# Performance work log

Hardware: AMD Instinct MI355X
Metric: run time of the kernel (lower is better)

Reference implementation:

```python
import jax, jax.numpy as jnp
import numpy as np

B, N, H = 8, 2048, 1024

def setup_inputs() -> dict:
    key = jax.random.key(0)
    ks = jax.random.split(key, 10)
    s = 1.0 / np.sqrt(2 * H)
    return {
        "sem": jax.random.normal(ks[0], (B, N, H), jnp.float32),
        "temp": jax.random.normal(ks[1], (B, N, H), jnp.float32),
        "Wq": jax.random.normal(ks[2], (2 * H, H), jnp.float32) * s,
        "bq": jnp.zeros((H,), jnp.float32),
        "Wk": jax.random.normal(ks[3], (2 * H, H), jnp.float32) * s,
        "bk": jnp.zeros((H,), jnp.float32),
        "Wv": jax.random.normal(ks[4], (2 * H, H), jnp.float32) * s,
        "bv": jnp.zeros((H,), jnp.float32),
        "Wg": jax.random.normal(ks[5], (2 * H, 1), jnp.float32) * s,
        "bg": jnp.zeros((1,), jnp.float32),
    }

def reference(sem, temp, Wq, bq, Wk, bk, Wv, bv, Wg, bg):
    combined = jnp.concatenate([sem, temp], axis=-1)          # [B,N,2H]
    Q = combined @ Wq + bq                                    # [B,N,H]
    K = combined @ Wk + bk
    V = combined @ Wv + bv
    scale = 1.0 / jnp.sqrt(jnp.asarray(Q.shape[-1], Q.dtype))
    scores = jnp.einsum('bqh,bkh->bqk', Q, K) * scale         # [B,N,N]
    attn = jax.nn.softmax(scores, axis=-1)
    gate = jax.nn.sigmoid(combined @ Wg + bg)                 # [B,N,1]
    attn_weights = attn * gate                                # row-wise gate
    fused = jnp.einsum('bqk,bkh->bqh', attn_weights, V)       # [B,N,H]
    return fused + sem, attn_weights.mean(axis=1)             # [B,N,H], [B,N]
```

## Files before the change

### kernel.cpp

```cpp
#include <hip/hip_runtime.h>
#include <stdint.h>
#include <math.h>

#define NB 8
#define NN 2048
#define HH 1024
#define K2 2048
#define MM 16384

typedef unsigned short u16;
typedef __attribute__((ext_vector_type(8))) short short8v;
typedef __attribute__((ext_vector_type(4))) float floatx4;

__device__ __forceinline__ float bf2f(u16 u) { return __uint_as_float(((unsigned)u) << 16); }
__device__ __forceinline__ u16 f2bf(float f) {
  unsigned u = __float_as_uint(f);
  unsigned r = (u + 0x7fffu + ((u >> 16) & 1u)) >> 16;
  return (u16)r;
}

__device__ __forceinline__ void async16(const void* g, void* lds) {
  __builtin_amdgcn_global_load_lds((const __attribute__((address_space(1))) void*)g,
                                   (__attribute__((address_space(3))) void*)lds,
                                   16, 0, 0);
}

__device__ __forceinline__ int xcd_swz(int bid, int nblk) {
  return (bid & 7) * (nblk >> 3) + (bid >> 3);
}

__device__ __forceinline__ void gemm256_core(const u16* __restrict__ A, int lda,
                                             const u16* __restrict__ Bt, int ldb,
                                             int rowA0, int rowB0, int K,
                                             u16* sA, u16* sB, floatx4 acc[8][4]) {
  const int t = threadIdx.x;
  const int w = t >> 6, l = t & 63;
  const int wr = w >> 2, wc = w & 3;

#pragma unroll
  for (int mi = 0; mi < 8; mi++)
#pragma unroll
    for (int ni = 0; ni < 4; ni++) { floatx4 z = {0.f,0.f,0.f,0.f}; acc[mi][ni] = z; }

  const int cS = ((t & 3) ^ ((t >> 3) & 3)) << 3;
  const u16* gA0 = A + (size_t)(rowA0 + (t >> 2)) * lda + cS;
  const u16* gA1 = A + (size_t)(rowA0 + 128 + (t >> 2)) * lda + cS;
  const u16* gB0 = Bt + (size_t)(rowB0 + (t >> 2)) * ldb + cS;
  const u16* gB1 = Bt + (size_t)(rowB0 + 128 + (t >> 2)) * ldb + cS;
  char* dA = (char*)sA + (w << 10) + (l << 4);
  char* dB = (char*)sB + (w << 10) + (l << 4);

  const int fr = l & 15;
  const int xr = (fr >> 1) & 3;
  const int ch = ((l >> 4) ^ xr) << 4;
  const int abase = (wr * 128 + fr) * 64 + ch;
  const int bbase = (wc * 64 + fr) * 64 + ch;

  const int NTt = K >> 5;

#define STG(bi, kt) { const int ko_ = (kt) << 5;                       \
    char* dA_ = dA + (bi) * 16384; char* dB_ = dB + (bi) * 16384;      \
    async16(gA0 + ko_, dA_);        async16(gA1 + ko_, dA_ + 8192);    \
    async16(gB0 + ko_, dB_);        async16(gB1 + ko_, dB_ + 8192); }

  STG(0, 0);
  STG(1, 1);

  int bc = 0, bs = 2;
  for (int tt = 0; tt < NTt; ++tt) {
    if (tt < NTt - 1) { asm volatile("s_waitcnt vmcnt(4)" ::: "memory"); }
    else              { asm volatile("s_waitcnt vmcnt(0)" ::: "memory"); }
    __builtin_amdgcn_s_barrier();
    if (tt + 2 < NTt) STG(bs, tt + 2);

    const char* a = (const char*)sA + bc * 16384;
    const char* b = (const char*)sB + bc * 16384;
    short8v bfr[4], afr[8];
#pragma unroll
    for (int ni = 0; ni < 4; ni++) bfr[ni] = *(const short8v*)(b + bbase + ni * 1024);
#pragma unroll
    for (int mi = 0; mi < 8; mi++) afr[mi] = *(const short8v*)(a + abase + mi * 1024);
    __builtin_amdgcn_s_setprio(1);
#pragma unroll
    for (int mi = 0; mi < 8; mi++)
#pragma unroll
      for (int ni = 0; ni < 4; ni++)
        acc[mi][ni] = __builtin_amdgcn_mfma_f32_16x16x32_bf16(afr[mi], bfr[ni], acc[mi][ni], 0, 0, 0);
    __builtin_amdgcn_s_setprio(0);
    bc = (bc == 2) ? 0 : bc + 1;
    bs = (bs == 2) ? 0 : bs + 1;
  }
#undef STG
}

__global__ void __launch_bounds__(256) k_prep_x(const float* __restrict__ sem,
                                                const float* __restrict__ temp,
                                                u16* __restrict__ X) {
  size_t i = (((size_t)blockIdx.x * 256) + threadIdx.x) << 2;
  int row = (int)(i >> 11);
  int col = (int)(i & 2047);
  const float* src = (col < 1024) ? (sem + (size_t)row * 1024 + col)
                                  : (temp + (size_t)row * 1024 + (col - 1024));
  float4 v = *(const float4*)src;
  ushort4 o;
  o.x = f2bf(v.x); o.y = f2bf(v.y); o.z = f2bf(v.z); o.w = f2bf(v.w);
  *(ushort4*)(X + i) = o;
}

__global__ void __launch_bounds__(256) k_transpose_w(const float* __restrict__ W,
                                                     u16* __restrict__ Wt) {
  __shared__ float s[32][33];
  int tile = blockIdx.x;
  int nt = tile & 31, kt = tile >> 5;
  int tx = threadIdx.x & 31, ty = threadIdx.x >> 5;
  int n0 = nt << 5, k0 = kt << 5;
#pragma unroll
  for (int j = 0; j < 32; j += 8)
    s[ty + j][tx] = W[(size_t)(k0 + ty + j) * 1024 + (n0 + tx)];
  __syncthreads();
#pragma unroll
  for (int j = 0; j < 32; j += 8)
    Wt[(size_t)(n0 + ty + j) * 2048 + (k0 + tx)] = f2bf(s[tx][ty + j]);
}

__global__ void __launch_bounds__(512, 2) k_proj_qkv(const u16* __restrict__ X,
                                                     const u16* __restrict__ Wt,
                                                     const float* __restrict__ bq,
                                                     const float* __restrict__ bk,
                                                     const float* __restrict__ bv,
                                                     u16* __restrict__ Qb,
                                                     u16* __restrict__ Kb,
                                                     u16* __restrict__ Vt) {
  __shared__ __align__(16) u16 sA[3 * 8192];
  __shared__ __align__(16) u16 sB[3 * 8192];
  int tile = xcd_swz(blockIdx.x, 768);
  int bm = tile / 12, bn = tile - bm * 12;
  floatx4 acc[8][4];
  gemm256_core(X, K2, Wt, K2, bm * 256, bn * 256, K2, sA, sB, acc);

  const int t = threadIdx.x, w = t >> 6, l = t & 63;
  const int wr = w >> 2, wc = w & 3;
  const int r0 = bm * 256 + wr * 128 + ((l >> 4) << 2);
  const int cg0 = bn * 256 + wc * 64 + (l & 15);
  const int which = bn >> 2;
  const float* bias = which == 0 ? bq : which == 1 ? bk : bv;
#pragma unroll
  for (int ni = 0; ni < 4; ni++) {
    int c1 = (cg0 + ni * 16) & 1023;
    float bvv = bias[c1];
#pragma unroll
    for (int mi = 0; mi < 8; mi++)
#pragma unroll
      for (int i = 0; i < 4; i++) {
        int rg = r0 + mi * 16 + i;
        u16 ob = f2bf(acc[mi][ni][i] + bvv);
        if (which == 0)      Qb[(size_t)rg * 1024 + c1] = ob;
        else if (which == 1) Kb[(size_t)rg * 1024 + c1] = ob;
        else                 Vt[((size_t)(rg >> 11) * 1024 + c1) * 2048 + (rg & 2047)] = ob;
      }
  }
}

__global__ void __launch_bounds__(256) k_gate(const u16* __restrict__ X, const float* __restrict__ Wg,
                                              const float* __restrict__ bg, float* __restrict__ gate) {
  int row = blockIdx.x * 4 + (threadIdx.x >> 6);
  int l = threadIdx.x & 63;
  const short* xr = (const short*)(X + (size_t)row * 2048);
  float s = 0.f;
#pragma unroll
  for (int i = 0; i < 4; i++) {
    int k = i * 512 + l * 8;
    short8v v = *(const short8v*)&xr[k];
#pragma unroll
    for (int j = 0; j < 8; j++) s += bf2f((u16)v[j]) * Wg[k + j];
  }
#pragma unroll
  for (int off = 32; off > 0; off >>= 1) s += __shfl_xor(s, off);
  if (l == 0) gate[row] = 1.f / (1.f + expf(-(s + bg[0])));
}

__global__ void __launch_bounds__(512, 2) k_scores(const u16* __restrict__ Q, const u16* __restrict__ Kb,
                                                   u16* __restrict__ E, float* __restrict__ lsum) {
  __shared__ __align__(16) u16 sA[3 * 8192];
  __shared__ __align__(16) u16 sB[3 * 8192];
  int tile = xcd_swz(blockIdx.x, 512);
  int b = tile >> 6, r = tile & 63, bm = r >> 3, bn = r & 7;
  const u16* A = Q + (size_t)b * NN * HH;
  const u16* Bt = Kb + (size_t)b * NN * HH;
  floatx4 acc[8][4];
  gemm256_core(A, HH, Bt, HH, bm * 256, bn * 256, HH, sA, sB, acc);

  u16* Eb = E + (size_t)b * NN * NN;
  float* lb = lsum + b * NN;
  const int t = threadIdx.x, w = t >> 6, l = t & 63;
  const int wr = w >> 2, wc = w & 3;
  const int q0 = bm * 256 + wr * 128 + ((l >> 4) << 2);
  const int k0c = bn * 256 + wc * 64 + (l & 15);
#pragma unroll
  for (int mi = 0; mi < 8; mi++)
#pragma unroll
    for (int i = 0; i < 4; i++) {
      int q = q0 + mi * 16 + i;
      float rs = 0.f;
#pragma unroll
      for (int ni = 0; ni < 4; ni++) {
        float e = expf(acc[mi][ni][i] * 0.03125f);
        Eb[(size_t)q * NN + k0c + ni * 16] = f2bf(e);
        rs += e;
      }
      rs += __shfl_xor(rs, 1);
      rs += __shfl_xor(rs, 2);
      rs += __shfl_xor(rs, 4);
      rs += __shfl_xor(rs, 8);
      if ((l & 15) == 0) atomicAdd(&lb[q], rs);
    }
}

__global__ void __launch_bounds__(512, 2) k_pv(const u16* __restrict__ E, const u16* __restrict__ Vt,
                                               const float* __restrict__ gate, const float* __restrict__ lsum,
                                               const float* __restrict__ sem, float* __restrict__ out) {
  __shared__ __align__(16) u16 sA[3 * 8192];
  __shared__ __align__(16) u16 sB[3 * 8192];
  int tile = xcd_swz(blockIdx.x, 256);
  int b = tile >> 5, r = tile & 31, bm = r >> 2, bn = r & 3;
  const u16* A = E + (size_t)b * NN * NN;
  const u16* Bt = Vt + (size_t)b * HH * NN;
  floatx4 acc[8][4];
  gemm256_core(A, NN, Bt, NN, bm * 256, bn * 256, NN, sA, sB, acc);

  const int t = threadIdx.x, w = t >> 6, l = t & 63;
  const int wr = w >> 2, wc = w & 3;
  const int q0 = bm * 256 + wr * 128 + ((l >> 4) << 2);
  const int h0 = bn * 256 + wc * 64 + (l & 15);
#pragma unroll
  for (int mi = 0; mi < 8; mi++)
#pragma unroll
    for (int i = 0; i < 4; i++) {
      int q = q0 + mi * 16 + i;
      size_t gq = (size_t)b * NN + q;
      float wq = gate[gq] / lsum[gq];
#pragma unroll
      for (int ni = 0; ni < 4; ni++) {
        int h = h0 + ni * 16;
        out[gq * HH + h] = acc[mi][ni][i] * wq + sem[gq * HH + h];
      }
    }
}

__global__ void __launch_bounds__(256) k_colmean(const u16* __restrict__ E, const float* __restrict__ gate,
                                                 const float* __restrict__ lsum, float* __restrict__ cm) {
  __shared__ float wsh[256];
  int bid = blockIdx.x;
  int b = bid >> 6, rest = bid & 63;
  int ks = rest >> 3, qc = rest & 7;
  int t = threadIdx.x;
  {
    size_t gq = (size_t)b * NN + qc * 256 + t;
    wsh[t] = gate[gq] / lsum[gq];
  }
  __syncthreads();
  int k = ks * 256 + t;
  const u16* Eb = E + ((size_t)b * NN + (size_t)qc * 256) * NN + k;
  float s = 0.f;
  for (int q = 0; q < 256; q++) s += wsh[q] * bf2f(Eb[(size_t)q * NN]);
  atomicAdd(&cm[b * NN + k], s * (1.f / 2048.f));
}

extern "C" void kernel_launch(void* const* d_in, const int* in_sizes, int n_in,
                              void* d_out, int out_size, void* d_ws, size_t ws_size,
                              hipStream_t stream) {
  const float* sem  = (const float*)d_in[0];
  const float* temp = (const float*)d_in[1];
  const float* Wq   = (const float*)d_in[2];
  const float* bq   = (const float*)d_in[3];
  const float* Wk   = (const float*)d_in[4];
  const float* bk   = (const float*)d_in[5];
  const float* Wv   = (const float*)d_in[6];
  const float* bv   = (const float*)d_in[7];
  const float* Wg   = (const float*)d_in[8];
  const float* bg   = (const float*)d_in[9];
  float* out = (float*)d_out;

  char* ws = (char*)d_ws;
  u16* X      = (u16*)ws;
  u16* E      = X;
  u16* WqkvT  = (u16*)(ws + 67108864);
  u16* Qb     = (u16*)(ws + 79691776);
  u16* Kb     = (u16*)(ws + 113246208);
  u16* Vt     = (u16*)(ws + 146800640);
  float* gate = (float*)(ws + 180355072);
  float* lsum = (float*)(ws + 180420608);

  hipMemsetAsync(lsum, 0, 65536, stream);
  hipMemsetAsync(out + 16777216, 0, 65536, stream);

  k_prep_x<<<32768, 256, 0, stream>>>(sem, temp, X);
  k_transpose_w<<<2048, 256, 0, stream>>>(Wq, WqkvT);
  k_transpose_w<<<2048, 256, 0, stream>>>(Wk, WqkvT + (size_t)1024 * 2048);
  k_transpose_w<<<2048, 256, 0, stream>>>(Wv, WqkvT + (size_t)2048 * 2048);
  k_proj_qkv<<<768, 512, 0, stream>>>(X, WqkvT, bq, bk, bv, Qb, Kb, Vt);
  k_gate<<<4096, 256, 0, stream>>>(X, Wg, bg, gate);
  k_scores<<<512, 512, 0, stream>>>(Qb, Kb, E, lsum);
  k_pv<<<256, 512, 0, stream>>>(E, Vt, gate, lsum, sem, out);
  k_colmean<<<512, 256, 0, stream>>>(E, gate, lsum, out + 16777216);
}
```

Before: 580.4 us.

## Switch GEMMs to 128x128 tiles with double buffering and fuse gate into prep

Replaces the 256x256, 512-thread, triple-buffered GEMM core with a 128x128, 256-thread, double-buffered core that has an extra barrier each iteration. The projection, scores and PV kernels get more, smaller blocks so more of them can run per CU. The gate computation moves into the bf16 conversion kernel and uses fp32 inputs, removing a separate pass over X. V is stored transposed with vectorized ushort4 writes. Smaller tiles lower per-block data reuse and raise global and LDS traffic per FLOP, and the shallower pipeline may expose load latency.

```diff
diff --git a/kernel.cpp b/kernel.cpp
--- a/kernel.cpp
+++ b/kernel.cpp
@@ -29,82 +29,101 @@
   return (bid & 7) * (nblk >> 3) + (bid >> 3);
 }
 
-__device__ __forceinline__ void gemm256_core(const u16* __restrict__ A, int lda,
+#define SBAR() __builtin_amdgcn_sched_barrier(0)
+
+__device__ __forceinline__ void gemm128_core(const u16* __restrict__ A, int lda,
                                              const u16* __restrict__ Bt, int ldb,
                                              int rowA0, int rowB0, int K,
-                                             u16* sA, u16* sB, floatx4 acc[8][4]) {
+                                             u16* sA, u16* sB, floatx4 acc[4][4]) {
   const int t = threadIdx.x;
   const int w = t >> 6, l = t & 63;
-  const int wr = w >> 2, wc = w & 3;
-
-#pragma unroll
-  for (int mi = 0; mi < 8; mi++)
+  const int wr = w >> 1, wc = w & 1;
+
+#pragma unroll
+  for (int mi = 0; mi < 4; mi++)
 #pragma unroll
     for (int ni = 0; ni < 4; ni++) { floatx4 z = {0.f,0.f,0.f,0.f}; acc[mi][ni] = z; }
 
-  const int cS = ((t & 3) ^ ((t >> 3) & 3)) << 3;
-  const u16* gA0 = A + (size_t)(rowA0 + (t >> 2)) * lda + cS;
-  const u16* gA1 = A + (size_t)(rowA0 + 128 + (t >> 2)) * lda + cS;
-  const u16* gB0 = Bt + (size_t)(rowB0 + (t >> 2)) * ldb + cS;
-  const u16* gB1 = Bt + (size_t)(rowB0 + 128 + (t >> 2)) * ldb + cS;
-  char* dA = (char*)sA + (w << 10) + (l << 4);
-  char* dB = (char*)sB + (w << 10) + (l << 4);
+  const int srow = l >> 2;
+  const int cs = (((l & 3) ^ ((l >> 3) & 3)) << 3);
+  const u16* gA0 = A + (size_t)(rowA0 + w * 32 + srow) * lda + cs;
+  const u16* gA1 = A + (size_t)(rowA0 + w * 32 + 16 + srow) * lda + cs;
+  const u16* gB0 = Bt + (size_t)(rowB0 + w * 32 + srow) * ldb + cs;
+  const u16* gB1 = Bt + (size_t)(rowB0 + w * 32 + 16 + srow) * ldb + cs;
+  char* dA = (char*)sA + w * 2048 + l * 16;
+  char* dB = (char*)sB + w * 2048 + l * 16;
 
   const int fr = l & 15;
-  const int xr = (fr >> 1) & 3;
-  const int ch = ((l >> 4) ^ xr) << 4;
-  const int abase = (wr * 128 + fr) * 64 + ch;
-  const int bbase = (wc * 64 + fr) * 64 + ch;
-
-  const int NTt = K >> 5;
-
-#define STG(bi, kt) { const int ko_ = (kt) << 5;                       \
-    char* dA_ = dA + (bi) * 16384; char* dB_ = dB + (bi) * 16384;      \
-    async16(gA0 + ko_, dA_);        async16(gA1 + ko_, dA_ + 8192);    \
-    async16(gB0 + ko_, dB_);        async16(gB1 + ko_, dB_ + 8192); }
-
-  STG(0, 0);
-  STG(1, 1);
-
-  int bc = 0, bs = 2;
-  for (int tt = 0; tt < NTt; ++tt) {
-    if (tt < NTt - 1) { asm volatile("s_waitcnt vmcnt(4)" ::: "memory"); }
-    else              { asm volatile("s_waitcnt vmcnt(0)" ::: "memory"); }
+  const int ch = (((l >> 4) ^ ((fr >> 1) & 3)) << 4);
+  const int abase = wr * 4096 + fr * 64 + ch;
+  const int bbase = wc * 4096 + fr * 64 + ch;
+
+  const int NT = K >> 5;
+
+#define STG128(bi, kt) { const int ko_ = (kt) << 5; const int bo_ = (bi) << 13; \
+    async16(gA0 + ko_, dA + bo_); async16(gA1 + ko_, dA + bo_ + 1024);          \
+    async16(gB0 + ko_, dB + bo_); async16(gB1 + ko_, dB + bo_ + 1024); }
+
+  STG128(0, 0);
+  for (int tt = 0; tt < NT; ++tt) {
+    const int bc = tt & 1;
+    if (tt + 1 < NT) {
+      STG128(bc ^ 1, tt + 1);
+      asm volatile("s_waitcnt vmcnt(4)" ::: "memory");
+    } else {
+      asm volatile("s_waitcnt vmcnt(0)" ::: "memory");
+    }
     __builtin_amdgcn_s_barrier();
-    if (tt + 2 < NTt) STG(bs, tt + 2);
-
-    const char* a = (const char*)sA + bc * 16384;
-    const char* b = (const char*)sB + bc * 16384;
-    short8v bfr[4], afr[8];
-#pragma unroll
-    for (int ni = 0; ni < 4; ni++) bfr[ni] = *(const short8v*)(b + bbase + ni * 1024);
-#pragma unroll
-    for (int mi = 0; mi < 8; mi++) afr[mi] = *(const short8v*)(a + abase + mi * 1024);
+
+    const char* a = (const char*)sA + (bc << 13);
+    const char* b = (const char*)sB + (bc << 13);
+    short8v af[4], bf[4];
+#pragma unroll
+    for (int mi = 0; mi < 4; mi++) af[mi] = *(const short8v*)(a + abase + mi * 1024);
+#pragma unroll
+    for (int ni = 0; ni < 4; ni++) bf[ni] = *(const short8v*)(b + bbase + ni * 1024);
     __builtin_amdgcn_s_setprio(1);
 #pragma unroll
-    for (int mi = 0; mi < 8; mi++)
+    for (int mi = 0; mi < 4; mi++)
 #pragma unroll
       for (int ni = 0; ni < 4; ni++)
-        acc[mi][ni] = __builtin_amdgcn_mfma_f32_16x16x32_bf16(afr[mi], bfr[ni], acc[mi][ni], 0, 0, 0);
+        acc[mi][ni] = __builtin_amdgcn_mfma_f32_16x16x32_bf16(af[mi], bf[ni], acc[mi][ni], 0, 0, 0);
     __builtin_amdgcn_s_setprio(0);
-    bc = (bc == 2) ? 0 : bc + 1;
-    bs = (bs == 2) ? 0 : bs + 1;
+    SBAR();
+    __builtin_amdgcn_s_barrier();
   }
-#undef STG
-}
-
-__global__ void __launch_bounds__(256) k_prep_x(const float* __restrict__ sem,
-                                                const float* __restrict__ temp,
-                                                u16* __restrict__ X) {
-  size_t i = (((size_t)blockIdx.x * 256) + threadIdx.x) << 2;
-  int row = (int)(i >> 11);
-  int col = (int)(i & 2047);
-  const float* src = (col < 1024) ? (sem + (size_t)row * 1024 + col)
-                                  : (temp + (size_t)row * 1024 + (col - 1024));
-  float4 v = *(const float4*)src;
-  ushort4 o;
-  o.x = f2bf(v.x); o.y = f2bf(v.y); o.z = f2bf(v.z); o.w = f2bf(v.w);
-  *(ushort4*)(X + i) = o;
+#undef STG128
+}
+
+__global__ void __launch_bounds__(256) k_prep_gate(const float* __restrict__ sem,
+                                                   const float* __restrict__ temp,
+                                                   const float* __restrict__ Wg,
+                                                   const float* __restrict__ bg,
+                                                   u16* __restrict__ X, float* __restrict__ gate) {
+  __shared__ float red[4];
+  int row = blockIdx.x;
+  int t = threadIdx.x, w = t >> 6, l = t & 63;
+  const float* s0 = sem + (size_t)row * 1024 + t * 4;
+  const float* t0 = temp + (size_t)row * 1024 + t * 4;
+  u16* xr = X + (size_t)row * 2048;
+  float4 a = *(const float4*)s0;
+  float4 b = *(const float4*)t0;
+  ushort4 oa = { f2bf(a.x), f2bf(a.y), f2bf(a.z), f2bf(a.w) };
+  ushort4 ob = { f2bf(b.x), f2bf(b.y), f2bf(b.z), f2bf(b.w) };
+  *(ushort4*)(xr + t * 4) = oa;
+  *(ushort4*)(xr + 1024 + t * 4) = ob;
+  float4 wa = *(const float4*)(Wg + t * 4);
+  float4 wb = *(const float4*)(Wg + 1024 + t * 4);
+  float s = a.x * wa.x + a.y * wa.y + a.z * wa.z + a.w * wa.w
+          + b.x * wb.x + b.y * wb.y + b.z * wb.z + b.w * wb.w;
+#pragma unroll
+  for (int off = 32; off > 0; off >>= 1) s += __shfl_xor(s, off);
+  if (l == 0) red[w] = s;
+  __syncthreads();
+  if (t == 0) {
+    float tot = red[0] + red[1] + red[2] + red[3] + bg[0];
+    gate[row] = 1.f / (1.f + expf(-tot));
+  }
 }
 
 __global__ void __launch_bounds__(256) k_transpose_w(const float* __restrict__ W,
@@ -123,7 +142,7 @@
     Wt[(size_t)(n0 + ty + j) * 2048 + (k0 + tx)] = f2bf(s[tx][ty + j]);
 }
 
-__global__ void __launch_bounds__(512, 2) k_proj_qkv(const u16* __restrict__ X,
+__global__ void __launch_bounds__(256, 3) k_proj_qkv(const u16* __restrict__ X,
                                                      const u16* __restrict__ Wt,
                                                      const float* __restrict__ bq,
                                                      const float* __restrict__ bk,
@@ -131,73 +150,67 @@
                                                      u16* __restrict__ Qb,
                                                      u16* __restrict__ Kb,
                                                      u16* __restrict__ Vt) {
-  __shared__ __align__(16) u16 sA[3 * 8192];
-  __shared__ __align__(16) u16 sB[3 * 8192];
-  int tile = xcd_swz(blockIdx.x, 768);
-  int bm = tile / 12, bn = tile - bm * 12;
-  floatx4 acc[8][4];
-  gemm256_core(X, K2, Wt, K2, bm * 256, bn * 256, K2, sA, sB, acc);
+  __shared__ __align__(16) u16 sA[2 * 4096];
+  __shared__ __align__(16) u16 sB[2 * 4096];
+  int tile = xcd_swz(blockIdx.x, 3072);
+  int bm = tile / 24, bn = tile - bm * 24;
+  floatx4 acc[4][4];
+  gemm128_core(X, K2, Wt, K2, bm * 128, bn * 128, K2, sA, sB, acc);
 
   const int t = threadIdx.x, w = t >> 6, l = t & 63;
-  const int wr = w >> 2, wc = w & 3;
-  const int r0 = bm * 256 + wr * 128 + ((l >> 4) << 2);
-  const int cg0 = bn * 256 + wc * 64 + (l & 15);
-  const int which = bn >> 2;
-  const float* bias = which == 0 ? bq : which == 1 ? bk : bv;
-#pragma unroll
-  for (int ni = 0; ni < 4; ni++) {
-    int c1 = (cg0 + ni * 16) & 1023;
-    float bvv = bias[c1];
-#pragma unroll
-    for (int mi = 0; mi < 8; mi++)
-#pragma unroll
-      for (int i = 0; i < 4; i++) {
-        int rg = r0 + mi * 16 + i;
-        u16 ob = f2bf(acc[mi][ni][i] + bvv);
-        if (which == 0)      Qb[(size_t)rg * 1024 + c1] = ob;
-        else if (which == 1) Kb[(size_t)rg * 1024 + c1] = ob;
-        else                 Vt[((size_t)(rg >> 11) * 1024 + c1) * 2048 + (rg & 2047)] = ob;
+  const int wr = w >> 1, wc = w & 1;
+  const int r0 = bm * 128 + wr * 64 + ((l >> 4) << 2);
+  const int c0 = (bn & 7) * 128 + wc * 64 + (l & 15);
+  const int which = bn >> 3;
+  if (which == 2) {
+#pragma unroll
+    for (int ni = 0; ni < 4; ni++) {
+      int h = c0 + ni * 16;
+      float bvv = bv[h];
+#pragma unroll
+      for (int mi = 0; mi < 4; mi++) {
+        int rg = r0 + mi * 16;
+        int b = rg >> 11, n = rg & 2047;
+        ushort4 o = { f2bf(acc[mi][ni][0] + bvv), f2bf(acc[mi][ni][1] + bvv),
+                      f2bf(acc[mi][ni][2] + bvv), f2bf(acc[mi][ni][3] + bvv) };
+        *(ushort4*)&Vt[((size_t)b * 1024 + h) * 2048 + n] = o;
       }
+    }
+  } else {
+    u16* Out = (which == 0) ? Qb : Kb;
+    const float* bias = (which == 0) ? bq : bk;
+#pragma unroll
+    for (int ni = 0; ni < 4; ni++) {
+      int c1 = c0 + ni * 16;
+      float bvv = bias[c1];
+#pragma unroll
+      for (int mi = 0; mi < 4; mi++)
+#pragma unroll
+        for (int i = 0; i < 4; i++)
+          Out[(size_t)(r0 + mi * 16 + i) * 1024 + c1] = f2bf(acc[mi][ni][i] + bvv);
+    }
   }
 }
 
-__global__ void __launch_bounds__(256) k_gate(const u16* __restrict__ X, const float* __restrict__ Wg,
-                                              const float* __restrict__ bg, float* __restrict__ gate) {
-  int row = blockIdx.x * 4 + (threadIdx.x >> 6);
-  int l = threadIdx.x & 63;
-  const short* xr = (const short*)(X + (size_t)row * 2048);
-  float s = 0.f;
-#pragma unroll
-  for (int i = 0; i < 4; i++) {
-    int k = i * 512 + l * 8;
-    short8v v = *(const short8v*)&xr[k];
-#pragma unroll
-    for (int j = 0; j < 8; j++) s += bf2f((u16)v[j]) * Wg[k + j];
-  }
-#pragma unroll
-  for (int off = 32; off > 0; off >>= 1) s += __shfl_xor(s, off);
-  if (l == 0) gate[row] = 1.f / (1.f + expf(-(s + bg[0])));
-}
-
-__global__ void __launch_bounds__(512, 2) k_scores(const u16* __restrict__ Q, const u16* __restrict__ Kb,
+__global__ void __launch_bounds__(256, 3) k_scores(const u16* __restrict__ Q, const u16* __restrict__ Kb,
                                                    u16* __restrict__ E, float* __restrict__ lsum) {
-  __shared__ __align__(16) u16 sA[3 * 8192];
-  __shared__ __align__(16) u16 sB[3 * 8192];
-  int tile = xcd_swz(blockIdx.x, 512);
-  int b = tile >> 6, r = tile & 63, bm = r >> 3, bn = r & 7;
+  __shared__ __align__(16) u16 sA[2 * 4096];
+  __shared__ __align__(16) u16 sB[2 * 4096];
+  int tile = xcd_swz(blockIdx.x, 2048);
+  int b = tile >> 8, r = tile & 255, bm = r >> 4, bn = r & 15;
   const u16* A = Q + (size_t)b * NN * HH;
   const u16* Bt = Kb + (size_t)b * NN * HH;
-  floatx4 acc[8][4];
-  gemm256_core(A, HH, Bt, HH, bm * 256, bn * 256, HH, sA, sB, acc);
+  floatx4 acc[4][4];
+  gemm128_core(A, HH, Bt, HH, bm * 128, bn * 128, HH, sA, sB, acc);
 
   u16* Eb = E + (size_t)b * NN * NN;
   float* lb = lsum + b * NN;
   const int t = threadIdx.x, w = t >> 6, l = t & 63;
-  const int wr = w >> 2, wc = w & 3;
-  const int q0 = bm * 256 + wr * 128 + ((l >> 4) << 2);
-  const int k0c = bn * 256 + wc * 64 + (l & 15);
-#pragma unroll
-  for (int mi = 0; mi < 8; mi++)
+  const int wr = w >> 1, wc = w & 1;
+  const int q0 = bm * 128 + wr * 64 + ((l >> 4) << 2);
+  const int k0c = bn * 128 + wc * 64 + (l & 15);
+#pragma unroll
+  for (int mi = 0; mi < 4; mi++)
 #pragma unroll
     for (int i = 0; i < 4; i++) {
       int q = q0 + mi * 16 + i;
@@ -216,24 +229,24 @@
     }
 }
 
-__global__ void __launch_bounds__(512, 2) k_pv(const u16* __restrict__ E, const u16* __restrict__ Vt,
+__global__ void __launch_bounds__(256, 3) k_pv(const u16* __restrict__ E, const u16* __restrict__ Vt,
                                                const float* __restrict__ gate, const float* __restrict__ lsum,
                                                const float* __restrict__ sem, float* __restrict__ out) {
-  __shared__ __align__(16) u16 sA[3 * 8192];
-  __shared__ __align__(16) u16 sB[3 * 8192];
-  int tile = xcd_swz(blockIdx.x, 256);
-  int b = tile >> 5, r = tile & 31, bm = r >> 2, bn = r & 3;
+  __shared__ __align__(16) u16 sA[2 * 4096];
+  __shared__ __align__(16) u16 sB[2 * 4096];
+  int tile = xcd_swz(blockIdx.x, 1024);
+  int b = tile >> 7, r = tile & 127, bm = r >> 3, bn = r & 7;
   const u16* A = E + (size_t)b * NN * NN;
   const u16* Bt = Vt + (size_t)b * HH * NN;
-  floatx4 acc[8][4];
-  gemm256_core(A, NN, Bt, NN, bm * 256, bn * 256, NN, sA, sB, acc);
+  floatx4 acc[4][4];
+  gemm128_core(A, NN, Bt, NN, bm * 128, bn * 128, NN, sA, sB, acc);
 
   const int t = threadIdx.x, w = t >> 6, l = t & 63;
-  const int wr = w >> 2, wc = w & 3;
-  const int q0 = bm * 256 + wr * 128 + ((l >> 4) << 2);
-  const int h0 = bn * 256 + wc * 64 + (l & 15);
-#pragma unroll
-  for (int mi = 0; mi < 8; mi++)
+  const int wr = w >> 1, wc = w & 1;
+  const int q0 = bm * 128 + wr * 64 + ((l >> 4) << 2);
+  const int h0 = bn * 128 + wc * 64 + (l & 15);
+#pragma unroll
+  for (int mi = 0; mi < 4; mi++)
 #pragma unroll
     for (int i = 0; i < 4; i++) {
       int q = q0 + mi * 16 + i;
@@ -294,13 +307,12 @@
   hipMemsetAsync(lsum, 0, 65536, stream);
   hipMemsetAsync(out + 16777216, 0, 65536, stream);
 
-  k_prep_x<<<32768, 256, 0, stream>>>(sem, temp, X);
+  k_prep_gate<<<16384, 256, 0, stream>>>(sem, temp, Wg, bg, X, gate);
   k_transpose_w<<<2048, 256, 0, stream>>>(Wq, WqkvT);
   k_transpose_w<<<2048, 256, 0, stream>>>(Wk, WqkvT + (size_t)1024 * 2048);
   k_transpose_w<<<2048, 256, 0, stream>>>(Wv, WqkvT + (size_t)2048 * 2048);
-  k_proj_qkv<<<768, 512, 0, stream>>>(X, WqkvT, bq, bk, bv, Qb, Kb, Vt);
-  k_gate<<<4096, 256, 0, stream>>>(X, Wg, bg, gate);
-  k_scores<<<512, 512, 0, stream>>>(Qb, Kb, E, lsum);
-  k_pv<<<256, 512, 0, stream>>>(E, Vt, gate, lsum, sem, out);
+  k_proj_qkv<<<3072, 256, 0, stream>>>(X, WqkvT, bq, bk, bv, Qb, Kb, Vt);
+  k_scores<<<2048, 256, 0, stream>>>(Qb, Kb, E, lsum);
+  k_pv<<<1024, 256, 0, stream>>>(E, Vt, gate, lsum, sem, out);
   k_colmean<<<512, 256, 0, stream>>>(E, gate, lsum, out + 16777216);
 }
```

Result: faster. 502.2 us (-13.5%).
